# Optimization experiments

Hardware: AMD Instinct MI355X
Metric: run time of the kernel (lower is better)

The kernel has to match this reference:

```python
import jax, jax.numpy as jnp
import numpy as np

N_NODES = 100000
N_EDGES = 1600000
N_GRAPHS = 5000
NODE_DIM = 16
EDGE_DIM = 16
HID = 20


def setup_inputs() -> dict:
    key = jax.random.key(0)
    ks = jax.random.split(key, 12)
    edge_index = jax.random.randint(ks[0], (2, N_EDGES), 0, N_NODES)
    node_attr = jax.random.normal(ks[1], (N_NODES, NODE_DIM), dtype=jnp.float32)
    edge_attr = jax.random.normal(ks[2], (N_EDGES, EDGE_DIM), dtype=jnp.float32)
    batch = jnp.sort(jax.random.randint(ks[3], (N_NODES,), 0, N_GRAPHS))
    s = 0.1
    W_msg = jax.random.normal(ks[4], (2 * NODE_DIM + EDGE_DIM, HID), dtype=jnp.float32) * s
    b_msg = jnp.zeros((HID,), dtype=jnp.float32)
    W1 = jax.random.normal(ks[5], (HID, 10), dtype=jnp.float32) * s
    b1 = jnp.zeros((10,), dtype=jnp.float32)
    W2 = jax.random.normal(ks[6], (10, 10), dtype=jnp.float32) * s
    b2 = jnp.zeros((10,), dtype=jnp.float32)
    W3 = jax.random.normal(ks[7], (10, 1), dtype=jnp.float32) * s
    b3 = jnp.zeros((1,), dtype=jnp.float32)
    return {"edge_index": edge_index, "node_attr": node_attr, "edge_attr": edge_attr,
            "batch": batch, "W_msg": W_msg, "b_msg": b_msg, "W1": W1, "b1": b1,
            "W2": W2, "b2": b2, "W3": W3, "b3": b3}


def reference(edge_index, node_attr, edge_attr, batch,
              W_msg, b_msg, W1, b1, W2, b2, W3, b3):
    src, dst = edge_index[0], edge_index[1]
    # MPL_1: gather -> linear -> relu -> scatter-sum to destination nodes
    feats = jnp.concatenate([node_attr[src], node_attr[dst], edge_attr], axis=-1)  # [E, 48]
    msg = jax.nn.relu(feats @ W_msg + b_msg)  # [E, 20]
    x = jax.ops.segment_sum(msg, dst, num_segments=N_NODES)  # [N, 20]
    # node MLP + graph pooling (segment_coo sum over batch) + graph MLP
    x = jax.nn.relu(x @ W1 + b1)  # [N, 10]
    g = jax.ops.segment_sum(x, batch, num_segments=N_GRAPHS)  # [G, 10]
    g = jax.nn.relu(g @ W2 + b2)
    return g @ W3 + b3  # [G, 1]
```

## Files before the change

### kernel.cpp

```cpp
#include <hip/hip_runtime.h>

constexpr int NN = 100000;
constexpr int NE = 1600000;
constexpr int NG = 5000;
constexpr int BKT = 64;
constexpr int NBKT = (NN + BKT - 1) / BKT;
constexpr int NB = 128;
constexpr int CHUNK = NE / NB;

typedef float v2f __attribute__((ext_vector_type(2)));

constexpr size_t OFF_G  = 0;
constexpr size_t OFF_BH = 50048;
constexpr size_t OFF_ST = OFF_BH + (size_t)NB * NBKT;
constexpr size_t OFF_PM = OFF_ST + NBKT + 1;
constexpr size_t OFF_SP = OFF_PM + NE;
constexpr size_t OFF_EP = ((OFF_SP + NE) + 15) & ~(size_t)15;
constexpr size_t NEED_WORDS = OFF_EP + (size_t)NE * 16;

__global__ __launch_bounds__(256) void k_hist(const int* __restrict__ ei,
                                              int* __restrict__ bh,
                                              float* __restrict__ g) {
  __shared__ int lh[NBKT];
  for (int i = threadIdx.x; i < NBKT; i += 256) lh[i] = 0;
  __syncthreads();
  const int* dstp = ei + NE;
  int s = blockIdx.x * CHUNK;
  for (int i = s + threadIdx.x; i < s + CHUNK; i += 256)
    atomicAdd(&lh[dstp[i] >> 6], 1);
  int gid = blockIdx.x * 256 + threadIdx.x;
  if (gid < 12500) ((float4*)g)[gid] = make_float4(0.f, 0.f, 0.f, 0.f);
  __syncthreads();
  int* out = bh + (size_t)blockIdx.x * NBKT;
  for (int k = threadIdx.x; k < NBKT; k += 256) out[k] = lh[k];
}

__global__ __launch_bounds__(256) void k_btot(const int* __restrict__ bh,
                                              int* __restrict__ starts) {
  int k = blockIdx.x * 256 + threadIdx.x;
  if (k >= NBKT) return;
  int tot = 0;
  for (int b = 0; b < NB; b += 4) {
    int a0 = bh[(size_t)(b    ) * NBKT + k];
    int a1 = bh[(size_t)(b + 1) * NBKT + k];
    int a2 = bh[(size_t)(b + 2) * NBKT + k];
    int a3 = bh[(size_t)(b + 3) * NBKT + k];
    tot += a0 + a1 + a2 + a3;
  }
  starts[k] = tot;
}

__global__ __launch_bounds__(1024) void k_sscan(int* __restrict__ starts) {
  __shared__ int s0[1024], s1[1024];
  int t = threadIdx.x;
  int k0 = 2 * t, k1 = 2 * t + 1;
  int tot0 = (k0 < NBKT) ? starts[k0] : 0;
  int tot1 = (k1 < NBKT) ? starts[k1] : 0;
  int ssum = tot0 + tot1;
  int* cur = s0; int* nxt = s1;
  cur[t] = ssum;
  __syncthreads();
  for (int off = 1; off < 1024; off <<= 1) {
    int v = cur[t];
    if (t >= off) v += cur[t - off];
    nxt[t] = v;
    __syncthreads();
    int* tmp = cur; cur = nxt; nxt = tmp;
  }
  int excl = cur[t] - ssum;
  if (k0 < NBKT) starts[k0] = excl;
  if (k1 <= NBKT) starts[k1] = excl + tot0;
}

__global__ __launch_bounds__(256) void k_bases(int* __restrict__ bh,
                                               const int* __restrict__ starts) {
  int k = blockIdx.x * 256 + threadIdx.x;
  if (k >= NBKT) return;
  int run = starts[k];
  for (int b = 0; b < NB; ++b) {
    size_t idx = (size_t)b * NBKT + k;
    int v = bh[idx];
    bh[idx] = run;
    run += v;
  }
}

template <bool PRE>
__global__ __launch_bounds__(256) void k_scatter(const int* __restrict__ ei,
                                                 const int* __restrict__ bh,
                                                 int* __restrict__ pm) {
  __shared__ int base[NBKT];
  __shared__ int cnt[NBKT];
  const int* row = bh + (size_t)blockIdx.x * NBKT;
  for (int k = threadIdx.x; k < NBKT; k += 256) { base[k] = row[k]; cnt[k] = 0; }
  __syncthreads();
  const int* dstp = ei + NE;
  int s = blockIdx.x * CHUNK;
  for (int i = s + threadIdx.x; i < s + CHUNK; i += 256) {
    int d = dstp[i];
    int k = d >> 6;
    int r = atomicAdd(&cnt[k], 1);
    int slot = base[k] + r;
    if (PRE) pm[i] = slot | ((d & 63) << 25);
    else     pm[slot] = i | ((d & 63) << 24);
  }
}

__global__ __launch_bounds__(256) void k_reorder(const int* __restrict__ ei,
                                                 const float* __restrict__ eattr,
                                                 const int* __restrict__ inv,
                                                 float* __restrict__ ep_,
                                                 int* __restrict__ srcp) {
  int gid = blockIdx.x * 256 + threadIdx.x;
  int e = gid >> 2, part = gid & 3;
  if (e >= NE) return;
  int iv = inv[e];
  int slot = iv & 0x1FFFFFF;
  float4 v = ((const float4*)eattr)[(size_t)e * 4 + part];
  ((float4*)ep_)[(size_t)slot * 4 + part] = v;
  if (part == 0) srcp[slot] = ei[e] | ((iv >> 25) << 24);
}

#define PK4(V, K0) \
  a0 = __builtin_elementwise_fma(v2f{(V).x, (V).x}, W[K0+0], a0); \
  a1 = __builtin_elementwise_fma(v2f{(V).y, (V).y}, W[K0+1], a1); \
  a2 = __builtin_elementwise_fma(v2f{(V).z, (V).z}, W[K0+2], a2); \
  a3 = __builtin_elementwise_fma(v2f{(V).w, (V).w}, W[K0+3], a3);

template <bool PRE>
__global__ __launch_bounds__(512, 1) void k_edge(
    const int* __restrict__ ei,
    const float* __restrict__ nattr,
    const float* __restrict__ eattr,
    const float* __restrict__ Wm,
    const float* __restrict__ bm,
    const int* __restrict__ batch,
    const float* __restrict__ W1,
    const float* __restrict__ b1,
    const int* __restrict__ pm,
    const int* __restrict__ starts,
    float* __restrict__ g) {
  __shared__ float xt[20 * 65];
  __shared__ float gb[64 * 10];
  __shared__ float4 wt4[250];
  __shared__ float4 us4[64 * 5];
  __shared__ float4 feat[8 * 54];
  __shared__ int s_se[2];
  __shared__ int s_bmin;
  int tid = threadIdx.x;
  for (int i = tid; i < 20 * 65; i += 512) xt[i] = 0.f;
  for (int i = tid; i < 640; i += 512) gb[i] = 0.f;
  if (tid < 240) {
    int j = tid / 24, t = tid - j * 24, k = 2 * t;
    wt4[j * 25 + t] = make_float4(Wm[k * 20 + 2 * j],       Wm[k * 20 + 2 * j + 1],
                                  Wm[(k + 1) * 20 + 2 * j], Wm[(k + 1) * 20 + 2 * j + 1]);
  }
  int nbase = blockIdx.x * BKT;
  if (tid < 256) {
    int dl = tid >> 2, part = tid & 3;
    int row = min(nbase + dl, NN - 1);
    us4[dl * 5 + part] = ((const float4*)nattr)[(size_t)row * 4 + part];
  }
  if (tid < 2) s_se[tid] = starts[blockIdx.x + tid];
  if (tid == 0) s_bmin = batch[nbase];
  __syncthreads();
  int is = s_se[0], ie = s_se[1];

  int wave = tid >> 6;
  int lane = tid & 63;
  int ep = lane / 10;
  int jp = lane - ep * 10;
  bool act = ep < 6;
  int epc = act ? ep : 0;

  v2f bj = {bm[2 * jp], bm[2 * jp + 1]};

  v2f W[48];
#pragma unroll
  for (int t = 0; t < 24; ++t) {
    float4 q = wt4[jp * 25 + t];
    W[2 * t]     = v2f{q.x, q.y};
    W[2 * t + 1] = v2f{q.z, q.w};
  }
#pragma unroll
  for (int k = 0; k < 48; ++k) asm volatile("" : "+v"(W[k]));

  int ce = lane >> 3, cpart = lane & 7;
  bool ldr = lane < 48;
  int esrc = (ldr ? ce : 0) * 10;
  int fbase = wave * 54;

  int base = is + wave * 6;
  if (PRE) {
    int sp0 = 0, sp1 = 0;
    float4 st = make_float4(0.f, 0.f, 0.f, 0.f);
    if (base < ie) {
      sp0 = pm[min(base + epc, ie - 1)];
      sp1 = (base + 48 < ie) ? pm[min(base + 48 + epc, ie - 1)] : sp0;
      int ss = __shfl(sp0, esrc) & 0xFFFFFF;
      if (ldr) {
        st = (cpart < 4)
          ? ((const float4*)eattr)[(size_t)min(base + ce, ie - 1) * 4 + cpart]
          : ((const float4*)nattr)[(size_t)ss * 4 + (cpart - 4)];
      }
    }
    while (base < ie) {
      if (ldr) feat[fbase + ce * 9 + cpart] = st;
      int ss = __shfl(sp1, esrc) & 0xFFFFFF;
      int sp2 = (base + 96 < ie) ? pm[min(base + 96 + epc, ie - 1)] : sp1;
      if (ldr) {
        st = (cpart < 4)
          ? ((const float4*)eattr)[(size_t)min(base + 48 + ce, ie - 1) * 4 + cpart]
          : ((const float4*)nattr)[(size_t)ss * 4 + (cpart - 4)];
      }
      int dl = (sp0 >> 24) & 63;
      int frow = fbase + ep * 9;
      float4 e0 = feat[frow + 0], e1 = feat[frow + 1], e2 = feat[frow + 2], e3 = feat[frow + 3];
      float4 n0 = feat[frow + 4], n1 = feat[frow + 5], n2 = feat[frow + 6], n3 = feat[frow + 7];
      float4 u0 = us4[dl * 5 + 0], u1 = us4[dl * 5 + 1], u2 = us4[dl * 5 + 2], u3 = us4[dl * 5 + 3];

      v2f a0 = {0.f, 0.f}, a1 = {0.f, 0.f}, a2 = {0.f, 0.f}, a3 = {0.f, 0.f};
      PK4(n0, 0)  PK4(n1, 4)  PK4(n2, 8)  PK4(n3, 12)
      PK4(u0, 16) PK4(u1, 20) PK4(u2, 24) PK4(u3, 28)
      PK4(e0, 32) PK4(e1, 36) PK4(e2, 40) PK4(e3, 44)
      v2f r = ((a0 + a1) + (a2 + a3)) + bj;

      bool valid = act && (base + epc < ie);
      float m0 = fmaxf(r.x, 0.f);
      float m1 = fmaxf(r.y, 0.f);
      if (valid && m0 > 0.f) atomicAdd(&xt[(2 * jp) * 65 + dl], m0);
      if (valid && m1 > 0.f) atomicAdd(&xt[(2 * jp + 1) * 65 + dl], m1);

      base += 48; sp0 = sp1; sp1 = sp2;
    }
  } else {
    int p0 = 0, p1 = 0, p2 = 0, svn = 0;
    float4 st = make_float4(0.f, 0.f, 0.f, 0.f);
    if (base < ie) {
      p0 = pm[min(base + epc, ie - 1)];
      p1 = (base + 48 < ie) ? pm[min(base + 48 + epc, ie - 1)] : p0;
      p2 = (base + 96 < ie) ? pm[min(base + 96 + epc, ie - 1)] : p1;
      int sv0 = ei[p0 & 0xFFFFFF];
      svn     = ei[p1 & 0xFFFFFF];
      int pp = __shfl(p0, esrc);
      int ss = __shfl(sv0, esrc);
      if (ldr) {
        st = (cpart < 4)
          ? ((const float4*)eattr)[(size_t)(pp & 0xFFFFFF) * 4 + cpart]
          : ((const float4*)nattr)[(size_t)ss * 4 + (cpart - 4)];
      }
    }
    while (base < ie) {
      if (ldr) feat[fbase + ce * 9 + cpart] = st;
      int pp = __shfl(p1, esrc);
      int ss = __shfl(svn, esrc);
      int p3 = (base + 144 < ie) ? pm[min(base + 144 + epc, ie - 1)] : p2;
      int svn2 = ei[p2 & 0xFFFFFF];
      if (ldr) {
        st = (cpart < 4)
          ? ((const float4*)eattr)[(size_t)(pp & 0xFFFFFF) * 4 + cpart]
          : ((const float4*)nattr)[(size_t)ss * 4 + (cpart - 4)];
      }
      int dl = (p0 >> 24) & 63;
      int frow = fbase + ep * 9;
      float4 e0 = feat[frow + 0], e1 = feat[frow + 1], e2 = feat[frow + 2], e3 = feat[frow + 3];
      float4 n0 = feat[frow + 4], n1 = feat[frow + 5], n2 = feat[frow + 6], n3 = feat[frow + 7];
      float4 u0 = us4[dl * 5 + 0], u1 = us4[dl * 5 + 1], u2 = us4[dl * 5 + 2], u3 = us4[dl * 5 + 3];

      v2f a0 = {0.f, 0.f}, a1 = {0.f, 0.f}, a2 = {0.f, 0.f}, a3 = {0.f, 0.f};
      PK4(n0, 0)  PK4(n1, 4)  PK4(n2, 8)  PK4(n3, 12)
      PK4(u0, 16) PK4(u1, 20) PK4(u2, 24) PK4(u3, 28)
      PK4(e0, 32) PK4(e1, 36) PK4(e2, 40) PK4(e3, 44)
      v2f r = ((a0 + a1) + (a2 + a3)) + bj;

      bool valid = act && (base + epc < ie);
      float m0 = fmaxf(r.x, 0.f);
      float m1 = fmaxf(r.y, 0.f);
      if (valid && m0 > 0.f) atomicAdd(&xt[(2 * jp) * 65 + dl], m0);
      if (valid && m1 > 0.f) atomicAdd(&xt[(2 * jp + 1) * 65 + dl], m1);

      base += 48; p0 = p1; p1 = p2; p2 = p3; svn = svn2;
    }
  }
  __syncthreads();

  int nn = min(BKT, NN - nbase);
  int bmin = s_bmin;
  if (tid < 64 && tid < nn) {
    int node = tid;
    float xi[20];
#pragma unroll
    for (int j = 0; j < 20; ++j) xi[j] = xt[j * 65 + node];
    float acc[10];
#pragma unroll
    for (int j = 0; j < 10; ++j) acc[j] = b1[j];
#pragma unroll
    for (int k = 0; k < 20; ++k) {
      float fk = xi[k];
#pragma unroll
      for (int j = 0; j < 10; ++j) acc[j] = fmaf(fk, W1[k * 10 + j], acc[j]);
    }
    int bn = batch[nbase + node];
    int d = bn - bmin;
    if (d < 64) {
#pragma unroll
      for (int j = 0; j < 10; ++j) {
        float m = fmaxf(acc[j], 0.f);
        if (m > 0.f) atomicAdd(&gb[d * 10 + j], m);
      }
    } else {
#pragma unroll
      for (int j = 0; j < 10; ++j) {
        float m = fmaxf(acc[j], 0.f);
        if (m > 0.f) unsafeAtomicAdd(&g[(size_t)bn * 10 + j], m);
      }
    }
  }
  __syncthreads();
  int glim = min(640, NG * 10 - bmin * 10);
  float* gp = g + (size_t)bmin * 10;
  for (int idx = tid; idx < glim; idx += 512) {
    float v = gb[idx];
    if (v != 0.f) unsafeAtomicAdd(&gp[idx], v);
  }
}

__global__ __launch_bounds__(256) void k_graph(
    const float* __restrict__ g,
    const float* __restrict__ W2, const float* __restrict__ b2,
    const float* __restrict__ W3, const float* __restrict__ b3,
    float* __restrict__ out) {
  int i = blockIdx.x * 256 + threadIdx.x;
  if (i >= NG) return;
  float gi[10];
  const float2* pg = (const float2*)(g + (size_t)i * 10);
#pragma unroll
  for (int k = 0; k < 5; ++k) { float2 v = pg[k]; gi[2*k] = v.x; gi[2*k+1] = v.y; }
  float o = b3[0];
#pragma unroll
  for (int j = 0; j < 10; ++j) {
    float a = b2[j];
#pragma unroll
    for (int k = 0; k < 10; ++k) a = fmaf(gi[k], W2[k * 10 + j], a);
    o = fmaf(fmaxf(a, 0.f), W3[j], o);
  }
  out[i] = o;
}

extern "C" void kernel_launch(void* const* d_in, const int* in_sizes, int n_in,
                              void* d_out, int out_size, void* d_ws, size_t ws_size,
                              hipStream_t stream) {
  const int*   ei    = (const int*)  d_in[0];
  const float* nattr = (const float*)d_in[1];
  const float* eattr = (const float*)d_in[2];
  const int*   batch = (const int*)  d_in[3];
  const float* Wm    = (const float*)d_in[4];
  const float* bm    = (const float*)d_in[5];
  const float* W1    = (const float*)d_in[6];
  const float* b1    = (const float*)d_in[7];
  const float* W2    = (const float*)d_in[8];
  const float* b2    = (const float*)d_in[9];
  const float* W3    = (const float*)d_in[10];
  const float* b3    = (const float*)d_in[11];

  float* g      = (float*)d_ws + OFF_G;
  int*   bh     = (int*)d_ws + OFF_BH;
  int*   starts = (int*)d_ws + OFF_ST;
  int*   pm     = (int*)d_ws + OFF_PM;
  int*   srcp   = (int*)d_ws + OFF_SP;
  float* ep_    = (float*)d_ws + OFF_EP;

  bool pre = ws_size >= NEED_WORDS * 4;

  constexpr int SCAN_BLKS = (NBKT + 255) / 256;

  k_hist   <<<NB, 256, 0, stream>>>(ei, bh, g);
  k_btot   <<<SCAN_BLKS, 256, 0, stream>>>(bh, starts);
  k_sscan  <<<1, 1024, 0, stream>>>(starts);
  k_bases  <<<SCAN_BLKS, 256, 0, stream>>>(bh, starts);
  if (pre) {
    k_scatter<true><<<NB, 256, 0, stream>>>(ei, bh, pm);
    k_reorder<<<(NE * 4 + 255) / 256, 256, 0, stream>>>(ei, eattr, pm, ep_, srcp);
    k_edge<true><<<NBKT, 512, 0, stream>>>(ei, nattr, ep_, Wm, bm, batch, W1, b1,
                                           srcp, starts, g);
  } else {
    k_scatter<false><<<NB, 256, 0, stream>>>(ei, bh, pm);
    k_edge<false><<<NBKT, 512, 0, stream>>>(ei, nattr, eattr, Wm, bm, batch, W1, b1,
                                            pm, starts, g);
  }
  k_graph  <<<(NG + 255) / 256, 256, 0, stream>>>(g, W2, b2, W3, b3, (float*)d_out);
}
```

Measured before the change: 440.2 us.

## Load edge features directly per lane and shrink edge blocks to 256 threads

The edge kernel drops the cooperative shared-memory staging of gathered edge and source-node features. Each lane now loads its own 64 bytes of edge and node attributes straight from global memory, and the software pipeline on the index array is kept. Blocks shrink from 512 to 256 threads with launch bounds (256,3), allowing more resident blocks per CU. This removes the LDS round trip and shuffles but replicates loads across the 10 lanes that share an edge, which raises L1/L2 traffic and may increase register pressure.

```diff
diff --git a/kernel.cpp b/kernel.cpp
--- a/kernel.cpp
+++ b/kernel.cpp
@@ -128,7 +128,7 @@
   a3 = __builtin_elementwise_fma(v2f{(V).w, (V).w}, W[K0+3], a3);
 
 template <bool PRE>
-__global__ __launch_bounds__(512, 1) void k_edge(
+__global__ __launch_bounds__(256, 3) void k_edge(
     const int* __restrict__ ei,
     const float* __restrict__ nattr,
     const float* __restrict__ eattr,
@@ -144,19 +144,18 @@
   __shared__ float gb[64 * 10];
   __shared__ float4 wt4[250];
   __shared__ float4 us4[64 * 5];
-  __shared__ float4 feat[8 * 54];
   __shared__ int s_se[2];
   __shared__ int s_bmin;
   int tid = threadIdx.x;
-  for (int i = tid; i < 20 * 65; i += 512) xt[i] = 0.f;
-  for (int i = tid; i < 640; i += 512) gb[i] = 0.f;
+  for (int i = tid; i < 20 * 65; i += 256) xt[i] = 0.f;
+  for (int i = tid; i < 640; i += 256) gb[i] = 0.f;
   if (tid < 240) {
     int j = tid / 24, t = tid - j * 24, k = 2 * t;
     wt4[j * 25 + t] = make_float4(Wm[k * 20 + 2 * j],       Wm[k * 20 + 2 * j + 1],
                                   Wm[(k + 1) * 20 + 2 * j], Wm[(k + 1) * 20 + 2 * j + 1]);
   }
   int nbase = blockIdx.x * BKT;
-  if (tid < 256) {
+  {
     int dl = tid >> 2, part = tid & 3;
     int row = min(nbase + dl, NN - 1);
     us4[dl * 5 + part] = ((const float4*)nattr)[(size_t)row * 4 + part];
@@ -185,102 +184,43 @@
 #pragma unroll
   for (int k = 0; k < 48; ++k) asm volatile("" : "+v"(W[k]));
 
-  int ce = lane >> 3, cpart = lane & 7;
-  bool ldr = lane < 48;
-  int esrc = (ldr ? ce : 0) * 10;
-  int fbase = wave * 54;
-
   int base = is + wave * 6;
-  if (PRE) {
-    int sp0 = 0, sp1 = 0;
-    float4 st = make_float4(0.f, 0.f, 0.f, 0.f);
-    if (base < ie) {
-      sp0 = pm[min(base + epc, ie - 1)];
-      sp1 = (base + 48 < ie) ? pm[min(base + 48 + epc, ie - 1)] : sp0;
-      int ss = __shfl(sp0, esrc) & 0xFFFFFF;
-      if (ldr) {
-        st = (cpart < 4)
-          ? ((const float4*)eattr)[(size_t)min(base + ce, ie - 1) * 4 + cpart]
-          : ((const float4*)nattr)[(size_t)ss * 4 + (cpart - 4)];
-      }
-    }
-    while (base < ie) {
-      if (ldr) feat[fbase + ce * 9 + cpart] = st;
-      int ss = __shfl(sp1, esrc) & 0xFFFFFF;
-      int sp2 = (base + 96 < ie) ? pm[min(base + 96 + epc, ie - 1)] : sp1;
-      if (ldr) {
-        st = (cpart < 4)
-          ? ((const float4*)eattr)[(size_t)min(base + 48 + ce, ie - 1) * 4 + cpart]
-          : ((const float4*)nattr)[(size_t)ss * 4 + (cpart - 4)];
-      }
-      int dl = (sp0 >> 24) & 63;
-      int frow = fbase + ep * 9;
-      float4 e0 = feat[frow + 0], e1 = feat[frow + 1], e2 = feat[frow + 2], e3 = feat[frow + 3];
-      float4 n0 = feat[frow + 4], n1 = feat[frow + 5], n2 = feat[frow + 6], n3 = feat[frow + 7];
-      float4 u0 = us4[dl * 5 + 0], u1 = us4[dl * 5 + 1], u2 = us4[dl * 5 + 2], u3 = us4[dl * 5 + 3];
-
-      v2f a0 = {0.f, 0.f}, a1 = {0.f, 0.f}, a2 = {0.f, 0.f}, a3 = {0.f, 0.f};
-      PK4(n0, 0)  PK4(n1, 4)  PK4(n2, 8)  PK4(n3, 12)
-      PK4(u0, 16) PK4(u1, 20) PK4(u2, 24) PK4(u3, 28)
-      PK4(e0, 32) PK4(e1, 36) PK4(e2, 40) PK4(e3, 44)
-      v2f r = ((a0 + a1) + (a2 + a3)) + bj;
-
-      bool valid = act && (base + epc < ie);
-      float m0 = fmaxf(r.x, 0.f);
-      float m1 = fmaxf(r.y, 0.f);
-      if (valid && m0 > 0.f) atomicAdd(&xt[(2 * jp) * 65 + dl], m0);
-      if (valid && m1 > 0.f) atomicAdd(&xt[(2 * jp + 1) * 65 + dl], m1);
-
-      base += 48; sp0 = sp1; sp1 = sp2;
-    }
-  } else {
-    int p0 = 0, p1 = 0, p2 = 0, svn = 0;
-    float4 st = make_float4(0.f, 0.f, 0.f, 0.f);
-    if (base < ie) {
-      p0 = pm[min(base + epc, ie - 1)];
-      p1 = (base + 48 < ie) ? pm[min(base + 48 + epc, ie - 1)] : p0;
-      p2 = (base + 96 < ie) ? pm[min(base + 96 + epc, ie - 1)] : p1;
-      int sv0 = ei[p0 & 0xFFFFFF];
-      svn     = ei[p1 & 0xFFFFFF];
-      int pp = __shfl(p0, esrc);
-      int ss = __shfl(sv0, esrc);
-      if (ldr) {
-        st = (cpart < 4)
-          ? ((const float4*)eattr)[(size_t)(pp & 0xFFFFFF) * 4 + cpart]
-          : ((const float4*)nattr)[(size_t)ss * 4 + (cpart - 4)];
-      }
-    }
-    while (base < ie) {
-      if (ldr) feat[fbase + ce * 9 + cpart] = st;
-      int pp = __shfl(p1, esrc);
-      int ss = __shfl(svn, esrc);
-      int p3 = (base + 144 < ie) ? pm[min(base + 144 + epc, ie - 1)] : p2;
-      int svn2 = ei[p2 & 0xFFFFFF];
-      if (ldr) {
-        st = (cpart < 4)
-          ? ((const float4*)eattr)[(size_t)(pp & 0xFFFFFF) * 4 + cpart]
-          : ((const float4*)nattr)[(size_t)ss * 4 + (cpart - 4)];
-      }
-      int dl = (p0 >> 24) & 63;
-      int frow = fbase + ep * 9;
-      float4 e0 = feat[frow + 0], e1 = feat[frow + 1], e2 = feat[frow + 2], e3 = feat[frow + 3];
-      float4 n0 = feat[frow + 4], n1 = feat[frow + 5], n2 = feat[frow + 6], n3 = feat[frow + 7];
-      float4 u0 = us4[dl * 5 + 0], u1 = us4[dl * 5 + 1], u2 = us4[dl * 5 + 2], u3 = us4[dl * 5 + 3];
-
-      v2f a0 = {0.f, 0.f}, a1 = {0.f, 0.f}, a2 = {0.f, 0.f}, a3 = {0.f, 0.f};
-      PK4(n0, 0)  PK4(n1, 4)  PK4(n2, 8)  PK4(n3, 12)
-      PK4(u0, 16) PK4(u1, 20) PK4(u2, 24) PK4(u3, 28)
-      PK4(e0, 32) PK4(e1, 36) PK4(e2, 40) PK4(e3, 44)
-      v2f r = ((a0 + a1) + (a2 + a3)) + bj;
-
-      bool valid = act && (base + epc < ie);
-      float m0 = fmaxf(r.x, 0.f);
-      float m1 = fmaxf(r.y, 0.f);
-      if (valid && m0 > 0.f) atomicAdd(&xt[(2 * jp) * 65 + dl], m0);
-      if (valid && m1 > 0.f) atomicAdd(&xt[(2 * jp + 1) * 65 + dl], m1);
-
-      base += 48; p0 = p1; p1 = p2; p2 = p3; svn = svn2;
-    }
+  int sp0 = 0, sp1 = 0, sp2 = 0, sv0 = 0;
+  if (base < ie) {
+    sp0 = pm[min(base + epc, ie - 1)];
+    sp1 = (base + 24 < ie) ? pm[min(base + 24 + epc, ie - 1)] : sp0;
+    sp2 = (base + 48 < ie) ? pm[min(base + 48 + epc, ie - 1)] : sp1;
+    if (!PRE) sv0 = ei[sp0 & 0xFFFFFF];
+  }
+  while (base < ie) {
+    int sp3 = (base + 72 < ie) ? pm[min(base + 72 + epc, ie - 1)] : sp2;
+    int svN = 0;
+    if (!PRE) svN = (base + 24 < ie) ? ei[sp1 & 0xFFFFFF] : sv0;
+
+    size_t eidx = PRE ? (size_t)min(base + epc, ie - 1)
+                      : (size_t)(sp0 & 0xFFFFFF);
+    int src = PRE ? (sp0 & 0xFFFFFF) : sv0;
+    const float4* pe = (const float4*)eattr + eidx * 4;
+    const float4* ps = (const float4*)nattr + (size_t)src * 4;
+    float4 e0 = pe[0], e1 = pe[1], e2 = pe[2], e3 = pe[3];
+    float4 n0 = ps[0], n1 = ps[1], n2 = ps[2], n3 = ps[3];
+    int dl = (sp0 >> 24) & 63;
+    float4 u0 = us4[dl * 5 + 0], u1 = us4[dl * 5 + 1];
+    float4 u2 = us4[dl * 5 + 2], u3 = us4[dl * 5 + 3];
+
+    v2f a0 = {0.f, 0.f}, a1 = {0.f, 0.f}, a2 = {0.f, 0.f}, a3 = {0.f, 0.f};
+    PK4(n0, 0)  PK4(n1, 4)  PK4(n2, 8)  PK4(n3, 12)
+    PK4(u0, 16) PK4(u1, 20) PK4(u2, 24) PK4(u3, 28)
+    PK4(e0, 32) PK4(e1, 36) PK4(e2, 40) PK4(e3, 44)
+    v2f r = ((a0 + a1) + (a2 + a3)) + bj;
+
+    bool valid = act && (base + epc < ie);
+    float m0 = fmaxf(r.x, 0.f);
+    float m1 = fmaxf(r.y, 0.f);
+    if (valid && m0 > 0.f) atomicAdd(&xt[(2 * jp) * 65 + dl], m0);
+    if (valid && m1 > 0.f) atomicAdd(&xt[(2 * jp + 1) * 65 + dl], m1);
+
+    base += 24; sp0 = sp1; sp1 = sp2; sp2 = sp3; sv0 = svN;
   }
   __syncthreads();
 
@@ -319,7 +259,7 @@
   __syncthreads();
   int glim = min(640, NG * 10 - bmin * 10);
   float* gp = g + (size_t)bmin * 10;
-  for (int idx = tid; idx < glim; idx += 512) {
+  for (int idx = tid; idx < glim; idx += 256) {
     float v = gb[idx];
     if (v != 0.f) unsafeAtomicAdd(&gp[idx], v);
   }
@@ -381,11 +321,11 @@
   if (pre) {
     k_scatter<true><<<NB, 256, 0, stream>>>(ei, bh, pm);
     k_reorder<<<(NE * 4 + 255) / 256, 256, 0, stream>>>(ei, eattr, pm, ep_, srcp);
-    k_edge<true><<<NBKT, 512, 0, stream>>>(ei, nattr, ep_, Wm, bm, batch, W1, b1,
+    k_edge<true><<<NBKT, 256, 0, stream>>>(ei, nattr, ep_, Wm, bm, batch, W1, b1,
                                            srcp, starts, g);
   } else {
     k_scatter<false><<<NB, 256, 0, stream>>>(ei, bh, pm);
-    k_edge<false><<<NBKT, 512, 0, stream>>>(ei, nattr, eattr, Wm, bm, batch, W1, b1,
+    k_edge<false><<<NBKT, 256, 0, stream>>>(ei, nattr, eattr, Wm, bm, batch, W1, b1,
                                             pm, starts, g);
   }
   k_graph  <<<(NG + 255) / 256, 256, 0, stream>>>(g, W2, b2, W3, b3, (float*)d_out);
```

New measurement: 382.7 us. 1.15x faster.
